# Optimization experiments

Measured on AMD Instinct MI355X. Metric: run time of the kernel, lower is better.

## Reference

```python
import jax, jax.numpy as jnp
import numpy as np

B, N, C, CODE, DIRB = 4, 321408, 3, 7, 2
K_PRE, K_POST = 1000, 300
IOU_THR, SCORE_THR, DIR_OFFSET = 0.5, 0.05, 0.0
POST_RANGE = np.array([0.0, -39.68, -5.0, 69.12, 39.68, 5.0], dtype=np.float32)


def setup_inputs() -> dict:
    key = jax.random.key(0)
    k1, k2, k3, k4 = jax.random.split(key, 4)
    box_preds = jax.random.normal(k1, (B, N, CODE), jnp.float32) * 0.3
    # shift logits down so sigmoid scores straddle the 0.05 threshold realistically
    cls_preds = jax.random.normal(k2, (B, N, C), jnp.float32) * 2.0 - 2.0
    dir_preds = jax.random.normal(k3, (B, N, DIRB), jnp.float32)
    ka, kb, kc = jax.random.split(k4, 3)
    xy = jax.random.uniform(ka, (N, 2), jnp.float32) * jnp.array([69.12, 79.36], jnp.float32) + jnp.array([0.0, -39.68], jnp.float32)
    z = jnp.full((N, 1), -1.0, jnp.float32)
    dims = jax.random.uniform(kb, (N, 3), jnp.float32, minval=1.0, maxval=4.0)
    rot = jax.random.randint(kc, (N, 1), 0, 2).astype(jnp.float32) * np.float32(np.pi / 2)
    anchors = jnp.concatenate([xy, z, dims, rot], axis=-1)
    return {"box_preds": box_preds, "cls_preds": cls_preds, "dir_preds": dir_preds, "anchors": anchors}


def _decode(deltas, anchors):
    # SECOND / PointPillars GroundBox3dCoder decode. anchors: [x,y,z,w,l,h,r]
    xa, ya, za, wa, la, ha, ra = (anchors[..., i] for i in range(7))
    xt, yt, zt, wt, lt, ht, rt = (deltas[..., i] for i in range(7))
    za = za + ha * 0.5
    diag = jnp.sqrt(la * la + wa * wa)
    xg = xt * diag + xa
    yg = yt * diag + ya
    zg = zt * ha + za
    wg = jnp.exp(wt) * wa
    lg = jnp.exp(lt) * la
    hg = jnp.exp(ht) * ha
    zg = zg - hg * 0.5
    rg = rt + ra
    return jnp.stack([xg, yg, zg, wg, lg, hg, rg], axis=-1)


def _nms_single(boxes7, scores, valid):
    # boxes_for_nms = box[:, [0,1,3,4,-1]] -> rotated (x,y,w,l,r); standup AABB of corners
    x, y, w, l, r = boxes7[:, 0], boxes7[:, 1], boxes7[:, 3], boxes7[:, 4], boxes7[:, 6]
    c, s = jnp.abs(jnp.cos(r)), jnp.abs(jnp.sin(r))
    hx = 0.5 * (w * c + l * s)   # half-extent of rotated corners along x
    hy = 0.5 * (w * s + l * c)
    x1, x2, y1, y2 = x - hx, x + hx, y - hy, y + hy
    area = (x2 - x1) * (y2 - y1)
    ix = jnp.clip(jnp.minimum(x2[:, None], x2[None, :]) - jnp.maximum(x1[:, None], x1[None, :]), 0.0)
    iy = jnp.clip(jnp.minimum(y2[:, None], y2[None, :]) - jnp.maximum(y1[:, None], y1[None, :]), 0.0)
    inter = ix * iy
    union = area[:, None] + area[None, :] - inter
    iou = jnp.where(union > 0, inter / jnp.maximum(union, 1e-12), 0.0)
    iou = jax.lax.stop_gradient(iou)
    idxs = jnp.arange(K_PRE)

    def body(keep, i):
        sup = keep[i] & (iou[i] > IOU_THR) & (idxs > i)
        return keep & ~sup, None

    keep, _ = jax.lax.scan(body, valid, idxs)
    rank = jnp.cumsum(keep) - 1                       # rank among kept (score order)
    pos = jnp.argsort(jnp.where(keep, rank, K_PRE))   # stable: kept-in-order first
    sel = pos[:K_POST]
    return sel, keep[sel]


def reference(box_preds, cls_preds, dir_preds, anchors):
    decoded = _decode(box_preds, anchors[None, :, :])          # [B,N,7]
    probs = jax.nn.sigmoid(cls_preds)                          # [B,N,C]
    top_scores = probs.max(axis=-1)
    top_labels = probs.argmax(axis=-1).astype(jnp.int32)
    dir_labels = dir_preds.argmax(axis=-1).astype(jnp.int32)
    valid = top_scores >= SCORE_THR
    sc_masked = jnp.where(valid, top_scores, -1.0)
    sc_k, idx = jax.lax.top_k(sc_masked, K_PRE)                # [B,K_PRE]
    boxes_k = jnp.take_along_axis(decoded, idx[..., None], axis=1)
    labels_k = jnp.take_along_axis(top_labels, idx, axis=1)
    dir_k = jnp.take_along_axis(dir_labels, idx, axis=1)
    valid_k = sc_k >= SCORE_THR
    sel, keep = jax.vmap(_nms_single)(boxes_k, sc_k, valid_k)  # [B,K_POST]
    boxes = jnp.take_along_axis(boxes_k, sel[..., None], axis=1)
    scores = jnp.take_along_axis(sc_k, sel, axis=1)
    labels = jnp.take_along_axis(labels_k, sel, axis=1)
    dirs = jnp.take_along_axis(dir_k, sel, axis=1)
    # direction flip: add pi where predicted direction disagrees with yaw sign
    opp = ((boxes[..., 6] - DIR_OFFSET) > 0) ^ (dirs == 1)
    r_fixed = boxes[..., 6] + jnp.where(opp, np.float32(np.pi), np.float32(0.0))
    boxes = jnp.concatenate([boxes[..., :6], r_fixed[..., None]], axis=-1)
    # post center-range filter
    lo = jnp.asarray(POST_RANGE[:3])
    hi = jnp.asarray(POST_RANGE[3:])
    in_range = jnp.all(boxes[..., :3] >= lo, axis=-1) & jnp.all(boxes[..., :3] <= hi, axis=-1)
    valid_out = keep & in_range
    boxes = jnp.where(valid_out[..., None], boxes, 0.0)
    scores = jnp.where(valid_out, scores, 0.0)
    labels = jnp.where(valid_out, labels, 0)
    return boxes, labels, scores, valid_out
```

## Files before the change

kernel.cpp:

```cpp
#include <hip/hip_runtime.h>
#include <stdint.h>

typedef unsigned long long u64;
typedef unsigned int u32;

#define BB 4
#define NN 321408
#define K_PRE 1000
#define K_POST 300
#define CAP 4096
#define NW 16
#define SCORE_THR 0.05f
#define IOU_THR 0.5f
#define SB 314
#define CH2 1024
#define NBINS 576
#define BIN0 0xBD4Cu
#define RED 8
#define RCH 40

__device__ __forceinline__ float sigm(float x) { return 1.0f / (1.0f + expf(-x)); }

__device__ __forceinline__ u32 mkkey(float mx) {
    float s = sigm(mx);
    return (s >= SCORE_THR) ? (__float_as_uint(s) | 0x80000000u) : 0u;
}

__global__ void k_score_hist(const float* __restrict__ cls, u32* __restrict__ key, u32* __restrict__ bh) {
    __shared__ u32 h1[NBINS], h2[NBINS];
    int bb = blockIdx.x, tid = threadIdx.x;
    int b = bb / SB, c = bb % SB;
    for (int i = tid; i < NBINS; i += 256) h1[i] = 0;
    __syncthreads();
    int a0 = c * CH2 + tid * 4;
    if (a0 < NN) {
        const float4* c4 = (const float4*)(cls + ((size_t)b * NN + a0) * 3);
        float4 v0 = c4[0], v1 = c4[1], v2 = c4[2];
        uint4 o;
        o.x = mkkey(fmaxf(v0.x, fmaxf(v0.y, v0.z)));
        o.y = mkkey(fmaxf(v0.w, fmaxf(v1.x, v1.y)));
        o.z = mkkey(fmaxf(v1.z, fmaxf(v1.w, v2.x)));
        o.w = mkkey(fmaxf(v2.y, fmaxf(v2.z, v2.w)));
        *((uint4*)(key + (size_t)b * NN + a0)) = o;
        if (o.x) atomicAdd(&h1[min((o.x >> 16) - BIN0, (u32)(NBINS - 1))], 1u);
        if (o.y) atomicAdd(&h1[min((o.y >> 16) - BIN0, (u32)(NBINS - 1))], 1u);
        if (o.z) atomicAdd(&h1[min((o.z >> 16) - BIN0, (u32)(NBINS - 1))], 1u);
        if (o.w) atomicAdd(&h1[min((o.w >> 16) - BIN0, (u32)(NBINS - 1))], 1u);
    }
    __syncthreads();
    u32* src = h1; u32* dst = h2;
    for (int off = 1; off < NBINS; off <<= 1) {
        for (int i = tid; i < NBINS; i += 256)
            dst[i] = src[i] + ((i + off < NBINS) ? src[i + off] : 0u);
        __syncthreads();
        u32* t = src; src = dst; dst = t;
    }
    for (int i = tid; i < NBINS; i += 256) bh[(size_t)bb * NBINS + i] = src[i];
}

__global__ __launch_bounds__(64) void k_red(const u32* __restrict__ bh, u32* __restrict__ part) {
    int blk = blockIdx.x, tid = threadIdx.x;
    int b = blk / (RED * 9);
    int r = (blk / 9) % RED;
    int g = blk % 9;
    int f = g * 64 + tid;
    int s0 = r * RCH, s1 = s0 + RCH; if (s1 > SB) s1 = SB;
    const u32* base = bh + (size_t)(b * SB + s0) * NBINS + f;
    u32 acc = 0;
    int n = s1 - s0;
    #pragma unroll 8
    for (int s = 0; s < n; ++s) acc += base[(size_t)s * NBINS];
    part[(size_t)(b * RED + r) * NBINS + f] = acc;
}

__global__ __launch_bounds__(512) void k_scanoff(const u32* __restrict__ part, const u32* __restrict__ bh,
                                                 u32* __restrict__ thr, u32* __restrict__ boff,
                                                 u32* __restrict__ cnt) {
    __shared__ u32 tot[NBINS];
    __shared__ u32 wt[8];
    __shared__ u32 sT, starg;
    int b = blockIdx.x, tid = threadIdx.x;
    for (int f = tid; f < NBINS; f += 512) {
        u32 x = 0;
        #pragma unroll
        for (int r = 0; r < RED; ++r) x += part[(size_t)(b * RED + r) * NBINS + f];
        tot[f] = x;
    }
    __syncthreads();
    if (tid == 0) {
        u32 tv = tot[0];
        starg = (tv < K_PRE) ? tv : K_PRE;
        if (starg == 0) { sT = 0x10000u; thr[b] = 0x10000u; }
    }
    __syncthreads();
    u32 target = starg;
    if (target > 0) {
        for (int f = tid; f < NBINS; f += 512) {
            u32 cge = tot[f];
            u32 cnx = (f + 1 < NBINS) ? tot[f + 1] : 0u;
            if (cge >= target && cnx < target) { sT = BIN0 + (u32)f; thr[b] = BIN0 + (u32)f; }
        }
    }
    __syncthreads();
    u32 v = 0;
    if (target > 0 && tid < SB) {
        u32 T = sT - BIN0;
        v = bh[(size_t)(b * SB + tid) * NBINS + T];
    }
    int lane = tid & 63, wv = tid >> 6;
    u32 x = v;
    #pragma unroll
    for (int o = 1; o < 64; o <<= 1) {
        u32 y = __shfl_up(x, o);
        if (lane >= o) x += y;
    }
    if (lane == 63) wt[wv] = x;
    __syncthreads();
    u32 pre = 0;
    #pragma unroll
    for (int w = 0; w < 7; ++w) pre += (w < wv) ? wt[w] : 0u;
    if (tid < SB) boff[b * SB + tid] = pre + x - v;
    if (tid == 511) cnt[b] = pre + x;
}

__global__ void k_scatter(const u32* __restrict__ key, const u32* __restrict__ thr,
                          const u32* __restrict__ boff, u64* __restrict__ cand) {
    __shared__ u32 wtot[4];
    int bb = blockIdx.x, tid = threadIdx.x;
    int b = bb / SB, c = bb % SB;
    u32 T = thr[b];
    int a0 = c * CH2 + tid * 4;
    uint4 kk = make_uint4(0u, 0u, 0u, 0u);
    if (a0 < NN) kk = *((const uint4*)(key + (size_t)b * NN + a0));
    u32 ks[4] = {kk.x, kk.y, kk.z, kk.w};
    u32 f[4];
    #pragma unroll
    for (int e = 0; e < 4; ++e) f[e] = (u32)((ks[e] != 0) && ((ks[e] >> 16) >= T));
    u32 tc = f[0] + f[1] + f[2] + f[3];
    int lane = tid & 63, wv = tid >> 6;
    u32 x = tc;
    #pragma unroll
    for (int o = 1; o < 64; o <<= 1) {
        u32 y = __shfl_up(x, o);
        if (lane >= o) x += y;
    }
    if (lane == 63) wtot[wv] = x;
    __syncthreads();
    u32 base = 0;
    u32 w0 = wtot[0], w1 = wtot[1], w2 = wtot[2];
    if (wv > 0) base += w0;
    if (wv > 1) base += w1;
    if (wv > 2) base += w2;
    u32 pos = boff[bb] + base + x - tc;
    u64* cb = cand + (size_t)b * CAP;
    #pragma unroll
    for (int e = 0; e < 4; ++e) {
        if (f[e]) {
            if (pos < CAP) cb[pos] = ((u64)(~ks[e]) << 32) | (u64)(a0 + e);
            ++pos;
        }
    }
}

__global__ __launch_bounds__(256) void k_rankdec(const u32* __restrict__ cnt, const u64* __restrict__ cand,
                                                 const float* __restrict__ boxp, const float* __restrict__ cls,
                                                 const float* __restrict__ dirp, const float* __restrict__ anch,
                                                 float* __restrict__ tks, u32* __restrict__ meta,
                                                 float* __restrict__ box7, float* __restrict__ cor) {
    __shared__ u64 ck[CAP];
    int blk = blockIdx.x, tid = threadIdx.x;
    int b = blk >> 4, rb = blk & 15;
    u32 nc = cnt[b]; if (nc > CAP) nc = CAP;
    int ci = rb * 256 + tid;
    if (rb * 256 >= (int)nc && rb * 256 >= K_PRE) return;
    const u64* cb = cand + (size_t)b * CAP;
    for (int i = tid; i < (int)nc; i += 256) ck[i] = cb[i];
    __syncthreads();

    int rank = -1; u32 idx = 0xFFFFFFFFu;
    if (ci < (int)nc) {
        u64 my = ck[ci];
        u32 r = 0;
        int j = 0;
        int nlim = (int)nc & ~15;
        for (; j < nlim; j += 16) {
            u64 v0 = ck[j+0], v1 = ck[j+1], v2 = ck[j+2], v3 = ck[j+3];
            u64 v4 = ck[j+4], v5 = ck[j+5], v6 = ck[j+6], v7 = ck[j+7];
            u64 v8 = ck[j+8], v9 = ck[j+9], va = ck[j+10], vb = ck[j+11];
            u64 vc = ck[j+12], vd = ck[j+13], ve = ck[j+14], vf = ck[j+15];
            r += (u32)(v0 < my) + (u32)(v1 < my) + (u32)(v2 < my) + (u32)(v3 < my)
               + (u32)(v4 < my) + (u32)(v5 < my) + (u32)(v6 < my) + (u32)(v7 < my)
               + (u32)(v8 < my) + (u32)(v9 < my) + (u32)(va < my) + (u32)(vb < my)
               + (u32)(vc < my) + (u32)(vd < my) + (u32)(ve < my) + (u32)(vf < my);
        }
        for (; j < (int)nc; ++j) r += (u32)(ck[j] < my);
        if (r < K_PRE) { rank = (int)r; idx = (u32)my; }
    } else if (ci < K_PRE) {
        rank = ci;
    }
    if (rank < 0) return;

    float ob[7] = {0,0,0,0,0,0,0};
    float c5[5] = {0,0,0,0,0};
    float sc = 0.f; u32 mt = 0;
    if (idx != 0xFFFFFFFFu) {
        const float* A = anch + (size_t)idx * 7;
        const float* D = boxp + ((size_t)b * NN + idx) * 7;
        float xa=A[0], ya=A[1], za=A[2], wa=A[3], la=A[4], ha=A[5], ra=A[6];
        float xt=D[0], yt=D[1], zt=D[2], wt=D[3], lt=D[4], ht=D[5], rt=D[6];
        za = za + ha * 0.5f;
        float diag = sqrtf(la * la + wa * wa);
        float xg = xt * diag + xa;
        float yg = yt * diag + ya;
        float zg = zt * ha + za;
        float wg = expf(wt) * wa;
        float lg = expf(lt) * la;
        float hg = expf(ht) * ha;
        zg = zg - hg * 0.5f;
        float rg = rt + ra;
        ob[0]=xg; ob[1]=yg; ob[2]=zg; ob[3]=wg; ob[4]=lg; ob[5]=hg; ob[6]=rg;
        float cr = fabsf(cosf(rg)), sr = fabsf(sinf(rg));
        float hx = 0.5f * (wg * cr + lg * sr);
        float hy = 0.5f * (wg * sr + lg * cr);
        float x1 = xg - hx, x2 = xg + hx, y1 = yg - hy, y2 = yg + hy;
        c5[0]=x1; c5[1]=x2; c5[2]=y1; c5[3]=y2; c5[4]=(x2-x1)*(y2-y1);
        const float* cc = cls + ((size_t)b * NN + idx) * 3;
        float p0 = sigm(cc[0]), p1 = sigm(cc[1]), p2 = sigm(cc[2]);
        int lbl = 0; float best = p0;
        if (p1 > best) { best = p1; lbl = 1; }
        if (p2 > best) { best = p2; lbl = 2; }
        sc = best;
        const float* dd = dirp + ((size_t)b * NN + idx) * 2;
        int dl = (dd[1] > dd[0]) ? 1 : 0;
        mt = (u32)lbl | ((u32)dl << 8) | (1u << 16);
    }
    size_t t = (size_t)b * K_PRE + rank;
    tks[t] = sc; meta[t] = mt;
    #pragma unroll
    for (int j = 0; j < 7; ++j) box7[t * 7 + j] = ob[j];
    #pragma unroll
    for (int j = 0; j < 5; ++j) cor[t * 5 + j] = c5[j];
}

__global__ __launch_bounds__(256) void k_maskT(const float* __restrict__ cor, u64* __restrict__ maskT) {
    __shared__ float s4[(K_PRE + 16) * 4];
    __shared__ float sA[K_PRE + 16];
    int blk = blockIdx.x;
    int b = blk / 63, jb = blk % 63;
    int tid = threadIdx.x;
    const float4* C4 = (const float4*)(cor + (size_t)b * K_PRE * 5);
    for (int q = tid; q < (K_PRE * 5) / 4; q += 256) {
        float4 v = C4[q];
        int t0 = q * 4;
        #pragma unroll
        for (int e = 0; e < 4; ++e) {
            int t = t0 + e;
            int i = t / 5, k = t - i * 5;
            float val = (e == 0) ? v.x : (e == 1) ? v.y : (e == 2) ? v.z : v.w;
            int ip = i + (i >> 6);
            if (k < 4) s4[ip * 4 + k] = val; else sA[ip] = val;
        }
    }
    __syncthreads();
    int w = tid & 15, jl = tid >> 4;
    int j = jb * 16 + jl;
    if (j >= K_PRE) return;
    int jp = j + (j >> 6);
    float x1 = s4[jp*4+0], x2 = s4[jp*4+1], y1 = s4[jp*4+2], y2 = s4[jp*4+3], ar = sA[jp];
    u64 m = 0;
    int i0 = w * 64;
    if (i0 < j) {
        int iend = j - i0; if (iend > 64) iend = 64;
        for (int ii = 0; ii < iend; ++ii) {
            int i = i0 + ii;
            int ip = i + (i >> 6);
            float4 bx = *(const float4*)&s4[ip * 4];
            float ai = sA[ip];
            float ix = fminf(x2, bx.y) - fmaxf(x1, bx.x); ix = fmaxf(ix, 0.f);
            float iy = fminf(y2, bx.w) - fmaxf(y1, bx.z); iy = fmaxf(iy, 0.f);
            float inter = ix * iy;
            float uni = ai + ar - inter;
            float iou = (uni > 0.f) ? inter / fmaxf(uni, 1e-12f) : 0.f;
            if (iou > IOU_THR) m |= (1ull << ii);
        }
    }
    maskT[((size_t)b * K_PRE + j) * NW + w] = m;
}

__global__ __launch_bounds__(256) void k_nms_out(const u32* __restrict__ meta, const float* __restrict__ box7,
                                                 const float* __restrict__ tks, const u64* __restrict__ maskT,
                                                 float* __restrict__ out) {
    int b = blockIdx.x; int tid = threadIdx.x;
    __shared__ u64 km_s[16];
    __shared__ int sel_s[K_POST];
    __shared__ int cnt_s;
    if (tid < 16) km_s[tid] = 0ull;
    __syncthreads();
    if (tid < 64) {
        int lane = tid;
        const u32* M = meta + b * K_PRE;
        int cnt = 0; bool done = false;
        for (int c = 0; c < 16; ++c) {
            if (done) break;
            int j = c * 64 + lane;
            int jc = (j < K_PRE) ? j : (K_PRE - 1);
            bool jvalid = (j < K_PRE) && ((M[jc] >> 16) & 1u);
            const u64* colp = maskT + ((size_t)b * K_PRE + jc) * NW;
            u64 cw = 0; u64 supacc = 0;
            #pragma unroll
            for (int w = 0; w < 16; ++w) {
                u64 cv = colp[w];
                supacc |= (cv & km_s[w]);
                if (w == c) cw = cv;
            }
            u64 active = __ballot(jvalid && (supacc == 0ull));
            u64 kmc = 0;
            while (active) {
                int i = __ffsll((unsigned long long)active) - 1;
                if (lane == 0) sel_s[cnt] = c * 64 + i;
                ++cnt;
                if (cnt >= K_POST) { done = true; break; }
                kmc |= (1ull << i);
                u64 supb = __ballot(((cw >> i) & 1ull) != 0ull);
                active &= ~supb;
                active &= ~(1ull << i);
            }
            if (lane == 0) km_s[c] = kmc;
        }
        if (lane == 0) cnt_s = cnt;
    }
    __syncthreads();
    int cnt = cnt_s;
    const u32* M = meta + b * K_PRE;
    const float* BX = box7 + (size_t)b * K_PRE * 7;
    const float* SS = tks + b * K_PRE;
    for (int p = tid; p < K_POST; p += 256) {
        float ob[7] = {0,0,0,0,0,0,0};
        float sc = 0.f, lb = 0.f, vd = 0.f;
        if (p < cnt) {
            int i = sel_s[p];
            float xg = BX[i*7+0], yg = BX[i*7+1], zg = BX[i*7+2];
            bool in_range = (xg >= 0.0f) && (xg <= 69.12f) &&
                            (yg >= -39.68f) && (yg <= 39.68f) &&
                            (zg >= -5.0f) && (zg <= 5.0f);
            if (in_range) {
                u32 mt = M[i];
                int dl = (mt >> 8) & 0xFF;
                float r = BX[i*7+6];
                bool opp = ((r > 0.0f) != (dl == 1));
                float rf = r + (opp ? 3.14159274f : 0.0f);
                ob[0]=xg; ob[1]=yg; ob[2]=zg; ob[3]=BX[i*7+3]; ob[4]=BX[i*7+4]; ob[5]=BX[i*7+5]; ob[6]=rf;
                sc = SS[i]; lb = (float)(mt & 0xFF); vd = 1.0f;
            }
        }
        size_t ro = (size_t)(b * K_POST + p);
        #pragma unroll
        for (int j = 0; j < 7; ++j) out[ro * 7 + j] = ob[j];
        out[(size_t)BB * K_POST * 7 + ro] = lb;
        out[(size_t)BB * K_POST * 8 + ro] = sc;
        out[(size_t)BB * K_POST * 9 + ro] = vd;
    }
}

extern "C" void kernel_launch(void* const* d_in, const int* in_sizes, int n_in,
                              void* d_out, int out_size, void* d_ws, size_t ws_size,
                              hipStream_t stream) {
    const float* boxp = (const float*)d_in[0];
    const float* cls  = (const float*)d_in[1];
    const float* dirp = (const float*)d_in[2];
    const float* anch = (const float*)d_in[3];
    float* out = (float*)d_out;

    char* p = (char*)d_ws;
    u32* key  = (u32*)p; p += (size_t)BB * NN * 4;
    u32* bh   = (u32*)p; p += (size_t)BB * SB * NBINS * 4;
    u32* part = (u32*)p; p += (size_t)BB * RED * NBINS * 4;
    u32* cnt  = (u32*)p; p += 256;
    u32* thr  = (u32*)p; p += 256;
    u32* boff = (u32*)p; p += (size_t)BB * SB * 4 + 256;
    u64* cand = (u64*)p; p += (size_t)BB * CAP * 8;
    float* tks = (float*)p; p += (size_t)BB * K_PRE * 4;
    u32* meta = (u32*)p; p += (size_t)BB * K_PRE * 4;
    float* box7 = (float*)p; p += (size_t)BB * K_PRE * 7 * 4;
    float* cor  = (float*)p; p += (size_t)BB * K_PRE * 5 * 4;
    u64* maskT = (u64*)p; p += (size_t)BB * K_PRE * NW * 8;

    k_score_hist<<<BB * SB, 256, 0, stream>>>(cls, key, bh);
    k_red<<<BB * RED * 9, 64, 0, stream>>>(bh, part);
    k_scanoff<<<BB, 512, 0, stream>>>(part, bh, thr, boff, cnt);
    k_scatter<<<BB * SB, 256, 0, stream>>>(key, thr, boff, cand);
    k_rankdec<<<BB * 16, 256, 0, stream>>>(cnt, cand, boxp, cls, dirp, anch, tks, meta, box7, cor);
    k_maskT<<<BB * 63, 256, 0, stream>>>(cor, maskT);
    k_nms_out<<<BB, 256, 0, stream>>>(meta, box7, tks, maskT, out);
}
```

Before: 87.91 us.

## Fuse all pipeline stages into one cooperative persistent kernel with grid syncs

```diff
diff --git a/kernel.cpp b/kernel.cpp
--- a/kernel.cpp
+++ b/kernel.cpp
@@ -1,5 +1,8 @@
 #include <hip/hip_runtime.h>
+#include <hip/hip_cooperative_groups.h>
 #include <stdint.h>
+
+namespace cg = cooperative_groups;
 
 typedef unsigned long long u64;
 typedef unsigned int u32;
@@ -18,12 +21,369 @@
 #define BIN0 0xBD4Cu
 #define RED 8
 #define RCH 40
+#define GRID 256
+#define TPB 256
 
 __device__ __forceinline__ float sigm(float x) { return 1.0f / (1.0f + expf(-x)); }
 
 __device__ __forceinline__ u32 mkkey(float mx) {
     float s = sigm(mx);
     return (s >= SCORE_THR) ? (__float_as_uint(s) | 0x80000000u) : 0u;
+}
+
+struct P1s { u32 h1[NBINS]; u32 h2[NBINS]; };
+struct P3s { u32 tot[NBINS]; u32 wt[4]; u32 sT; u32 starg; };
+struct P4s { u32 wtot[4]; };
+struct P5s { u64 ck[CAP]; };
+struct P6s { float s4[(K_PRE + 16) * 4]; float sA[K_PRE + 16]; };
+struct P7s { u64 km[16]; int sel[K_POST]; int cnt_s; };
+union SmemU { P1s p1; P3s p3; P4s p4; P5s p5; P6s p6; P7s p7; };
+
+__global__ void __launch_bounds__(TPB) k_mega(const float* __restrict__ boxp, const float* __restrict__ cls,
+                                              const float* __restrict__ dirp, const float* __restrict__ anch,
+                                              float* __restrict__ out, char* __restrict__ ws) {
+    __shared__ SmemU sm;
+    cg::grid_group gg = cg::this_grid();
+    int bid = blockIdx.x, tid = threadIdx.x;
+    int lane = tid & 63, wv = tid >> 6;
+
+    char* p = ws;
+    u32* key  = (u32*)p; p += (size_t)BB * NN * 4;
+    u32* bh   = (u32*)p; p += (size_t)BB * SB * NBINS * 4;
+    u32* part = (u32*)p; p += (size_t)BB * RED * NBINS * 4;
+    u32* cnt  = (u32*)p; p += 256;
+    u32* thr  = (u32*)p; p += 256;
+    u32* boff = (u32*)p; p += (size_t)BB * SB * 4 + 256;
+    u64* cand = (u64*)p; p += (size_t)BB * CAP * 8;
+    float* tks = (float*)p; p += (size_t)BB * K_PRE * 4;
+    u32* meta = (u32*)p; p += (size_t)BB * K_PRE * 4;
+    float* box7 = (float*)p; p += (size_t)BB * K_PRE * 7 * 4;
+    float* cor  = (float*)p; p += (size_t)BB * K_PRE * 5 * 4;
+    u64* maskT = (u64*)p;
+
+    for (int task = bid; task < BB * SB; task += GRID) {
+        int b = task / SB, c = task % SB;
+        for (int i = tid; i < NBINS; i += TPB) sm.p1.h1[i] = 0;
+        __syncthreads();
+        int a0 = c * CH2 + tid * 4;
+        if (a0 < NN) {
+            const float4* c4 = (const float4*)(cls + ((size_t)b * NN + a0) * 3);
+            float4 v0 = c4[0], v1 = c4[1], v2 = c4[2];
+            uint4 o;
+            o.x = mkkey(fmaxf(v0.x, fmaxf(v0.y, v0.z)));
+            o.y = mkkey(fmaxf(v0.w, fmaxf(v1.x, v1.y)));
+            o.z = mkkey(fmaxf(v1.z, fmaxf(v1.w, v2.x)));
+            o.w = mkkey(fmaxf(v2.y, fmaxf(v2.z, v2.w)));
+            *((uint4*)(key + (size_t)b * NN + a0)) = o;
+            if (o.x) atomicAdd(&sm.p1.h1[min((o.x >> 16) - BIN0, (u32)(NBINS - 1))], 1u);
+            if (o.y) atomicAdd(&sm.p1.h1[min((o.y >> 16) - BIN0, (u32)(NBINS - 1))], 1u);
+            if (o.z) atomicAdd(&sm.p1.h1[min((o.z >> 16) - BIN0, (u32)(NBINS - 1))], 1u);
+            if (o.w) atomicAdd(&sm.p1.h1[min((o.w >> 16) - BIN0, (u32)(NBINS - 1))], 1u);
+        }
+        __syncthreads();
+        u32* src = sm.p1.h1; u32* dst = sm.p1.h2;
+        for (int off = 1; off < NBINS; off <<= 1) {
+            for (int i = tid; i < NBINS; i += TPB)
+                dst[i] = src[i] + ((i + off < NBINS) ? src[i + off] : 0u);
+            __syncthreads();
+            u32* t = src; src = dst; dst = t;
+        }
+        for (int i = tid; i < NBINS; i += TPB) bh[(size_t)task * NBINS + i] = src[i];
+        __syncthreads();
+    }
+    gg.sync();
+
+    if (bid < BB * RED * 3) {
+        int b = bid / (RED * 3), r = (bid / 3) % RED, g = bid % 3;
+        int f = g * 256 + tid;
+        if (f < NBINS) {
+            int s0 = r * RCH, s1 = s0 + RCH; if (s1 > SB) s1 = SB;
+            const u32* base = bh + (size_t)(b * SB + s0) * NBINS + f;
+            u32 acc = 0; int n = s1 - s0;
+            #pragma unroll 8
+            for (int s = 0; s < n; ++s) acc += base[(size_t)s * NBINS];
+            part[(size_t)(b * RED + r) * NBINS + f] = acc;
+        }
+    }
+    gg.sync();
+
+    if (bid < BB) {
+        int b = bid;
+        for (int f = tid; f < NBINS; f += TPB) {
+            u32 x = 0;
+            #pragma unroll
+            for (int r = 0; r < RED; ++r) x += part[(size_t)(b * RED + r) * NBINS + f];
+            sm.p3.tot[f] = x;
+        }
+        __syncthreads();
+        if (tid == 0) {
+            u32 tv = sm.p3.tot[0];
+            sm.p3.starg = (tv < K_PRE) ? tv : K_PRE;
+            if (sm.p3.starg == 0) { sm.p3.sT = 0x10000u; thr[b] = 0x10000u; }
+        }
+        __syncthreads();
+        u32 target = sm.p3.starg;
+        if (target > 0) {
+            for (int f = tid; f < NBINS; f += TPB) {
+                u32 cge = sm.p3.tot[f];
+                u32 cnx = (f + 1 < NBINS) ? sm.p3.tot[f + 1] : 0u;
+                if (cge >= target && cnx < target) { sm.p3.sT = BIN0 + (u32)f; thr[b] = BIN0 + (u32)f; }
+            }
+        }
+        __syncthreads();
+        u32 T = sm.p3.sT;
+        u32 vA = 0, vB = 0;
+        if (target > 0) {
+            if (tid < SB) vA = bh[(size_t)(b * SB + tid) * NBINS + (T - BIN0)];
+            if (tid + 256 < SB) vB = bh[(size_t)(b * SB + tid + 256) * NBINS + (T - BIN0)];
+        }
+        u32 x = vA;
+        #pragma unroll
+        for (int o = 1; o < 64; o <<= 1) { u32 y = __shfl_up(x, o); if (lane >= o) x += y; }
+        if (lane == 63) sm.p3.wt[wv] = x;
+        __syncthreads();
+        u32 preA = 0, totA;
+        { u32 w0 = sm.p3.wt[0], w1 = sm.p3.wt[1], w2 = sm.p3.wt[2], w3 = sm.p3.wt[3];
+          if (wv > 0) preA += w0; if (wv > 1) preA += w1; if (wv > 2) preA += w2;
+          totA = w0 + w1 + w2 + w3; }
+        __syncthreads();
+        u32 xb = vB;
+        #pragma unroll
+        for (int o = 1; o < 64; o <<= 1) { u32 y = __shfl_up(xb, o); if (lane >= o) xb += y; }
+        if (lane == 63) sm.p3.wt[wv] = xb;
+        __syncthreads();
+        u32 preB = 0, totB;
+        { u32 w0 = sm.p3.wt[0], w1 = sm.p3.wt[1], w2 = sm.p3.wt[2], w3 = sm.p3.wt[3];
+          if (wv > 0) preB += w0; if (wv > 1) preB += w1; if (wv > 2) preB += w2;
+          totB = w0 + w1 + w2 + w3; }
+        if (tid < SB) boff[b * SB + tid] = preA + x - vA;
+        if (tid + 256 < SB) boff[b * SB + tid + 256] = totA + preB + xb - vB;
+        if (tid == 0) cnt[b] = totA + totB;
+    }
+    gg.sync();
+
+    for (int task = bid; task < BB * SB; task += GRID) {
+        int b = task / SB, c = task % SB;
+        u32 T = thr[b];
+        int a0 = c * CH2 + tid * 4;
+        uint4 kk = make_uint4(0u, 0u, 0u, 0u);
+        if (a0 < NN) kk = *((const uint4*)(key + (size_t)b * NN + a0));
+        u32 ks[4] = {kk.x, kk.y, kk.z, kk.w};
+        u32 f[4];
+        #pragma unroll
+        for (int e = 0; e < 4; ++e) f[e] = (u32)((ks[e] != 0) && ((ks[e] >> 16) >= T));
+        u32 tc = f[0] + f[1] + f[2] + f[3];
+        u32 x = tc;
+        #pragma unroll
+        for (int o = 1; o < 64; o <<= 1) { u32 y = __shfl_up(x, o); if (lane >= o) x += y; }
+        if (lane == 63) sm.p4.wtot[wv] = x;
+        __syncthreads();
+        u32 base = 0;
+        { u32 w0 = sm.p4.wtot[0], w1 = sm.p4.wtot[1], w2 = sm.p4.wtot[2];
+          if (wv > 0) base += w0; if (wv > 1) base += w1; if (wv > 2) base += w2; }
+        u32 pos = boff[task] + base + x - tc;
+        u64* cb = cand + (size_t)b * CAP;
+        #pragma unroll
+        for (int e = 0; e < 4; ++e) {
+            if (f[e]) {
+                if (pos < CAP) cb[pos] = ((u64)(~ks[e]) << 32) | (u64)(a0 + e);
+                ++pos;
+            }
+        }
+        __syncthreads();
+    }
+    gg.sync();
+
+    {
+        int b = bid >> 6, g = bid & 63;
+        u32 nc = cnt[b]; if (nc > CAP) nc = CAP;
+        int ci0 = g * 64;
+        bool active = (ci0 < (int)nc) || (ci0 < K_PRE);
+        if (active) {
+            const u64* cb = cand + (size_t)b * CAP;
+            for (int i = tid; i < (int)nc; i += TPB) sm.p5.ck[i] = cb[i];
+            __syncthreads();
+            int rank = -1; u32 idx = 0xFFFFFFFFu;
+            if (tid < 64) {
+                int ci = ci0 + tid;
+                if (ci < (int)nc) {
+                    u64 my = sm.p5.ck[ci];
+                    u32 r = 0;
+                    int j = 0, nlim = (int)nc & ~15;
+                    for (; j < nlim; j += 16) {
+                        u64 v0 = sm.p5.ck[j+0], v1 = sm.p5.ck[j+1], v2 = sm.p5.ck[j+2], v3 = sm.p5.ck[j+3];
+                        u64 v4 = sm.p5.ck[j+4], v5 = sm.p5.ck[j+5], v6 = sm.p5.ck[j+6], v7 = sm.p5.ck[j+7];
+                        u64 v8 = sm.p5.ck[j+8], v9 = sm.p5.ck[j+9], va = sm.p5.ck[j+10], vb = sm.p5.ck[j+11];
+                        u64 vc = sm.p5.ck[j+12], vd = sm.p5.ck[j+13], ve = sm.p5.ck[j+14], vf = sm.p5.ck[j+15];
+                        r += (u32)(v0 < my) + (u32)(v1 < my) + (u32)(v2 < my) + (u32)(v3 < my)
+                           + (u32)(v4 < my) + (u32)(v5 < my) + (u32)(v6 < my) + (u32)(v7 < my)
+                           + (u32)(v8 < my) + (u32)(v9 < my) + (u32)(va < my) + (u32)(vb < my)
+                           + (u32)(vc < my) + (u32)(vd < my) + (u32)(ve < my) + (u32)(vf < my);
+                    }
+                    for (; j < (int)nc; ++j) r += (u32)(sm.p5.ck[j] < my);
+                    if (r < K_PRE) { rank = (int)r; idx = (u32)my; }
+                } else if (ci < K_PRE) {
+                    rank = ci;
+                }
+            }
+            if (rank >= 0) {
+                float ob[7] = {0,0,0,0,0,0,0};
+                float c5[5] = {0,0,0,0,0};
+                float sc = 0.f; u32 mt = 0;
+                if (idx != 0xFFFFFFFFu) {
+                    const float* A = anch + (size_t)idx * 7;
+                    const float* D = boxp + ((size_t)b * NN + idx) * 7;
+                    float xa=A[0], ya=A[1], za=A[2], wa=A[3], la=A[4], ha=A[5], ra=A[6];
+                    float xt=D[0], yt=D[1], zt=D[2], wt2=D[3], lt=D[4], ht=D[5], rt=D[6];
+                    za = za + ha * 0.5f;
+                    float diag = sqrtf(la * la + wa * wa);
+                    float xg = xt * diag + xa;
+                    float yg = yt * diag + ya;
+                    float zg = zt * ha + za;
+                    float wg = expf(wt2) * wa;
+                    float lg = expf(lt) * la;
+                    float hg = expf(ht) * ha;
+                    zg = zg - hg * 0.5f;
+                    float rg = rt + ra;
+                    ob[0]=xg; ob[1]=yg; ob[2]=zg; ob[3]=wg; ob[4]=lg; ob[5]=hg; ob[6]=rg;
+                    float cr = fabsf(cosf(rg)), sr = fabsf(sinf(rg));
+                    float hx = 0.5f * (wg * cr + lg * sr);
+                    float hy = 0.5f * (wg * sr + lg * cr);
+                    float x1 = xg - hx, x2 = xg + hx, y1 = yg - hy, y2 = yg + hy;
+                    c5[0]=x1; c5[1]=x2; c5[2]=y1; c5[3]=y2; c5[4]=(x2-x1)*(y2-y1);
+                    const float* cc = cls + ((size_t)b * NN + idx) * 3;
+                    float p0 = sigm(cc[0]), p1 = sigm(cc[1]), p2 = sigm(cc[2]);
+                    int lbl = 0; float best = p0;
+                    if (p1 > best) { best = p1; lbl = 1; }
+                    if (p2 > best) { best = p2; lbl = 2; }
+                    sc = best;
+                    const float* dd = dirp + ((size_t)b * NN + idx) * 2;
+                    int dl = (dd[1] > dd[0]) ? 1 : 0;
+                    mt = (u32)lbl | ((u32)dl << 8) | (1u << 16);
+                }
+                size_t t = (size_t)b * K_PRE + rank;
+                tks[t] = sc; meta[t] = mt;
+                #pragma unroll
+                for (int j = 0; j < 7; ++j) box7[t * 7 + j] = ob[j];
+                #pragma unroll
+                for (int j = 0; j < 5; ++j) cor[t * 5 + j] = c5[j];
+            }
+        }
+    }
+    gg.sync();
+
+    if (bid < BB * 63) {
+        int b = bid / 63, jb = bid % 63;
+        const float4* C4 = (const float4*)(cor + (size_t)b * K_PRE * 5);
+        for (int q = tid; q < (K_PRE * 5) / 4; q += TPB) {
+            float4 v = C4[q];
+            int t0 = q * 4;
+            #pragma unroll
+            for (int e = 0; e < 4; ++e) {
+                int t = t0 + e;
+                int i = t / 5, k = t - i * 5;
+                float val = (e == 0) ? v.x : (e == 1) ? v.y : (e == 2) ? v.z : v.w;
+                int ip = i + (i >> 6);
+                if (k < 4) sm.p6.s4[ip * 4 + k] = val; else sm.p6.sA[ip] = val;
+            }
+        }
+        __syncthreads();
+        int w = tid & 15, jl = tid >> 4;
+        int j = jb * 16 + jl;
+        if (j < K_PRE) {
+            int jp = j + (j >> 6);
+            float x1 = sm.p6.s4[jp*4+0], x2 = sm.p6.s4[jp*4+1];
+            float y1 = sm.p6.s4[jp*4+2], y2 = sm.p6.s4[jp*4+3], ar = sm.p6.sA[jp];
+            u64 m = 0;
+            int i0 = w * 64;
+            if (i0 < j) {
+                int iend = j - i0; if (iend > 64) iend = 64;
+                for (int ii = 0; ii < iend; ++ii) {
+                    int i = i0 + ii;
+                    int ip = i + (i >> 6);
+                    float4 bx = *(const float4*)&sm.p6.s4[ip * 4];
+                    float ai = sm.p6.sA[ip];
+                    float ix = fminf(x2, bx.y) - fmaxf(x1, bx.x); ix = fmaxf(ix, 0.f);
+                    float iy = fminf(y2, bx.w) - fmaxf(y1, bx.z); iy = fmaxf(iy, 0.f);
+                    float inter = ix * iy;
+                    float uni = ai + ar - inter;
+                    float iou = (uni > 0.f) ? inter / fmaxf(uni, 1e-12f) : 0.f;
+                    if (iou > IOU_THR) m |= (1ull << ii);
+                }
+            }
+            maskT[((size_t)b * K_PRE + j) * NW + w] = m;
+        }
+    }
+    gg.sync();
+
+    if (bid < BB) {
+        int b = bid;
+        if (tid < 16) sm.p7.km[tid] = 0ull;
+        __syncthreads();
+        if (tid < 64) {
+            int c2 = 0; bool done = false;
+            const u32* M = meta + b * K_PRE;
+            for (int c = 0; c < 16; ++c) {
+                if (done) break;
+                int j = c * 64 + lane;
+                int jc = (j < K_PRE) ? j : (K_PRE - 1);
+                bool jvalid = (j < K_PRE) && ((M[jc] >> 16) & 1u);
+                const u64* colp = maskT + ((size_t)b * K_PRE + jc) * NW;
+                u64 cw = 0; u64 supacc = 0;
+                #pragma unroll
+                for (int w = 0; w < 16; ++w) {
+                    u64 cv = colp[w];
+                    supacc |= (cv & sm.p7.km[w]);
+                    if (w == c) cw = cv;
+                }
+                u64 active2 = __ballot(jvalid && (supacc == 0ull));
+                u64 kmc = 0;
+                while (active2) {
+                    int i = __ffsll((unsigned long long)active2) - 1;
+                    if (lane == 0) sm.p7.sel[c2] = c * 64 + i;
+                    ++c2;
+                    if (c2 >= K_POST) { done = true; break; }
+                    kmc |= (1ull << i);
+                    u64 supb = __ballot(((cw >> i) & 1ull) != 0ull);
+                    active2 &= ~supb;
+                    active2 &= ~(1ull << i);
+                }
+                if (lane == 0) sm.p7.km[c] = kmc;
+            }
+            if (lane == 0) sm.p7.cnt_s = c2;
+        }
+        __syncthreads();
+        int kept = sm.p7.cnt_s;
+        const u32* M = meta + b * K_PRE;
+        const float* BX = box7 + (size_t)b * K_PRE * 7;
+        const float* SS = tks + b * K_PRE;
+        for (int pp = tid; pp < K_POST; pp += TPB) {
+            float ob[7] = {0,0,0,0,0,0,0};
+            float sc = 0.f, lb = 0.f, vd = 0.f;
+            if (pp < kept) {
+                int i = sm.p7.sel[pp];
+                float xg = BX[i*7+0], yg = BX[i*7+1], zg = BX[i*7+2];
+                bool in_range = (xg >= 0.0f) && (xg <= 69.12f) &&
+                                (yg >= -39.68f) && (yg <= 39.68f) &&
+                                (zg >= -5.0f) && (zg <= 5.0f);
+                if (in_range) {
+                    u32 mt = M[i];
+                    int dl = (mt >> 8) & 0xFF;
+                    float r = BX[i*7+6];
+                    bool opp = ((r > 0.0f) != (dl == 1));
+                    float rf = r + (opp ? 3.14159274f : 0.0f);
+                    ob[0]=xg; ob[1]=yg; ob[2]=zg; ob[3]=BX[i*7+3]; ob[4]=BX[i*7+4]; ob[5]=BX[i*7+5]; ob[6]=rf;
+                    sc = SS[i]; lb = (float)(mt & 0xFF); vd = 1.0f;
+                }
+            }
+            size_t ro = (size_t)(b * K_POST + pp);
+            #pragma unroll
+            for (int j = 0; j < 7; ++j) out[ro * 7 + j] = ob[j];
+            out[(size_t)BB * K_POST * 7 + ro] = lb;
+            out[(size_t)BB * K_POST * 8 + ro] = sc;
+            out[(size_t)BB * K_POST * 9 + ro] = vd;
+        }
+    }
 }
 
 __global__ void k_score_hist(const float* __restrict__ cls, u32* __restrict__ key, u32* __restrict__ bh) {
@@ -60,14 +420,11 @@
 
 __global__ __launch_bounds__(64) void k_red(const u32* __restrict__ bh, u32* __restrict__ part) {
     int blk = blockIdx.x, tid = threadIdx.x;
-    int b = blk / (RED * 9);
-    int r = (blk / 9) % RED;
-    int g = blk % 9;
+    int b = blk / (RED * 9); int r = (blk / 9) % RED; int g = blk % 9;
     int f = g * 64 + tid;
     int s0 = r * RCH, s1 = s0 + RCH; if (s1 > SB) s1 = SB;
     const u32* base = bh + (size_t)(b * SB + s0) * NBINS + f;
-    u32 acc = 0;
-    int n = s1 - s0;
+    u32 acc = 0; int n = s1 - s0;
     #pragma unroll 8
     for (int s = 0; s < n; ++s) acc += base[(size_t)s * NBINS];
     part[(size_t)(b * RED + r) * NBINS + f] = acc;
@@ -103,17 +460,11 @@
     }
     __syncthreads();
     u32 v = 0;
-    if (target > 0 && tid < SB) {
-        u32 T = sT - BIN0;
-        v = bh[(size_t)(b * SB + tid) * NBINS + T];
-    }
+    if (target > 0 && tid < SB) v = bh[(size_t)(b * SB + tid) * NBINS + (sT - BIN0)];
     int lane = tid & 63, wv = tid >> 6;
     u32 x = v;
     #pragma unroll
-    for (int o = 1; o < 64; o <<= 1) {
-        u32 y = __shfl_up(x, o);
-        if (lane >= o) x += y;
-    }
+    for (int o = 1; o < 64; o <<= 1) { u32 y = __shfl_up(x, o); if (lane >= o) x += y; }
     if (lane == 63) wt[wv] = x;
     __syncthreads();
     u32 pre = 0;
@@ -140,10 +491,7 @@
     int lane = tid & 63, wv = tid >> 6;
     u32 x = tc;
     #pragma unroll
-    for (int o = 1; o < 64; o <<= 1) {
-        u32 y = __shfl_up(x, o);
-        if (lane >= o) x += y;
-    }
+    for (int o = 1; o < 64; o <<= 1) { u32 y = __shfl_up(x, o); if (lane >= o) x += y; }
     if (lane == 63) wtot[wv] = x;
     __syncthreads();
     u32 base = 0;
@@ -176,13 +524,11 @@
     const u64* cb = cand + (size_t)b * CAP;
     for (int i = tid; i < (int)nc; i += 256) ck[i] = cb[i];
     __syncthreads();
-
     int rank = -1; u32 idx = 0xFFFFFFFFu;
     if (ci < (int)nc) {
         u64 my = ck[ci];
         u32 r = 0;
-        int j = 0;
-        int nlim = (int)nc & ~15;
+        int j = 0, nlim = (int)nc & ~15;
         for (; j < nlim; j += 16) {
             u64 v0 = ck[j+0], v1 = ck[j+1], v2 = ck[j+2], v3 = ck[j+3];
             u64 v4 = ck[j+4], v5 = ck[j+5], v6 = ck[j+6], v7 = ck[j+7];
@@ -199,7 +545,6 @@
         rank = ci;
     }
     if (rank < 0) return;
-
     float ob[7] = {0,0,0,0,0,0,0};
     float c5[5] = {0,0,0,0,0};
     float sc = 0.f; u32 mt = 0;
@@ -370,26 +715,32 @@
     const float* dirp = (const float*)d_in[2];
     const float* anch = (const float*)d_in[3];
     float* out = (float*)d_out;
-
-    char* p = (char*)d_ws;
-    u32* key  = (u32*)p; p += (size_t)BB * NN * 4;
-    u32* bh   = (u32*)p; p += (size_t)BB * SB * NBINS * 4;
-    u32* part = (u32*)p; p += (size_t)BB * RED * NBINS * 4;
-    u32* cnt  = (u32*)p; p += 256;
-    u32* thr  = (u32*)p; p += 256;
-    u32* boff = (u32*)p; p += (size_t)BB * SB * 4 + 256;
-    u64* cand = (u64*)p; p += (size_t)BB * CAP * 8;
-    float* tks = (float*)p; p += (size_t)BB * K_PRE * 4;
-    u32* meta = (u32*)p; p += (size_t)BB * K_PRE * 4;
-    float* box7 = (float*)p; p += (size_t)BB * K_PRE * 7 * 4;
-    float* cor  = (float*)p; p += (size_t)BB * K_PRE * 5 * 4;
-    u64* maskT = (u64*)p; p += (size_t)BB * K_PRE * NW * 8;
-
-    k_score_hist<<<BB * SB, 256, 0, stream>>>(cls, key, bh);
-    k_red<<<BB * RED * 9, 64, 0, stream>>>(bh, part);
-    k_scanoff<<<BB, 512, 0, stream>>>(part, bh, thr, boff, cnt);
-    k_scatter<<<BB * SB, 256, 0, stream>>>(key, thr, boff, cand);
-    k_rankdec<<<BB * 16, 256, 0, stream>>>(cnt, cand, boxp, cls, dirp, anch, tks, meta, box7, cor);
-    k_maskT<<<BB * 63, 256, 0, stream>>>(cor, maskT);
-    k_nms_out<<<BB, 256, 0, stream>>>(meta, box7, tks, maskT, out);
-}
+    char* ws = (char*)d_ws;
+
+    void* args[] = { (void*)&boxp, (void*)&cls, (void*)&dirp, (void*)&anch, (void*)&out, (void*)&ws };
+    hipError_t err = hipLaunchCooperativeKernel((const void*)k_mega, dim3(GRID), dim3(TPB),
+                                                (void**)args, 0, stream);
+    if (err != hipSuccess) {
+        char* p = ws;
+        u32* key  = (u32*)p; p += (size_t)BB * NN * 4;
+        u32* bh   = (u32*)p; p += (size_t)BB * SB * NBINS * 4;
+        u32* part = (u32*)p; p += (size_t)BB * RED * NBINS * 4;
+        u32* cnt  = (u32*)p; p += 256;
+        u32* thr  = (u32*)p; p += 256;
+        u32* boff = (u32*)p; p += (size_t)BB * SB * 4 + 256;
+        u64* cand = (u64*)p; p += (size_t)BB * CAP * 8;
+        float* tks = (float*)p; p += (size_t)BB * K_PRE * 4;
+        u32* meta = (u32*)p; p += (size_t)BB * K_PRE * 4;
+        float* box7 = (float*)p; p += (size_t)BB * K_PRE * 7 * 4;
+        float* cor  = (float*)p; p += (size_t)BB * K_PRE * 5 * 4;
+        u64* maskT = (u64*)p;
+
+        k_score_hist<<<BB * SB, 256, 0, stream>>>(cls, key, bh);
+        k_red<<<BB * RED * 9, 64, 0, stream>>>(bh, part);
+        k_scanoff<<<BB, 512, 0, stream>>>(part, bh, thr, boff, cnt);
+        k_scatter<<<BB * SB, 256, 0, stream>>>(key, thr, boff, cand);
+        k_rankdec<<<BB * 16, 256, 0, stream>>>(cnt, cand, boxp, cls, dirp, anch, tks, meta, box7, cor);
+        k_maskT<<<BB * 63, 256, 0, stream>>>(cor, maskT);
+        k_nms_out<<<BB, 256, 0, stream>>>(meta, box7, tks, maskT, out);
+    }
+}
```

New measurement: 259.8 us. 2.96x slower.

## Fuse threshold scan and bucket-offset prefix into scatter kernel

Applied to the files above, without the earlier changes.

```diff
diff --git a/kernel.cpp b/kernel.cpp
--- a/kernel.cpp
+++ b/kernel.cpp
@@ -73,71 +73,54 @@
     part[(size_t)(b * RED + r) * NBINS + f] = acc;
 }
 
-__global__ __launch_bounds__(512) void k_scanoff(const u32* __restrict__ part, const u32* __restrict__ bh,
-                                                 u32* __restrict__ thr, u32* __restrict__ boff,
-                                                 u32* __restrict__ cnt) {
+__global__ __launch_bounds__(256) void k_scatterT(const u32* __restrict__ key, const u32* __restrict__ part,
+                                                  const u32* __restrict__ bh, u32* __restrict__ cnt,
+                                                  u64* __restrict__ cand) {
     __shared__ u32 tot[NBINS];
-    __shared__ u32 wt[8];
-    __shared__ u32 sT, starg;
-    int b = blockIdx.x, tid = threadIdx.x;
-    for (int f = tid; f < NBINS; f += 512) {
+    __shared__ u32 wtot[4];
+    __shared__ u32 sTf;
+    int bb = blockIdx.x, tid = threadIdx.x;
+    int b = bb / SB, c = bb % SB;
+    int lane = tid & 63, wv = tid >> 6;
+    for (int f = tid; f < NBINS; f += 256) {
         u32 x = 0;
         #pragma unroll
         for (int r = 0; r < RED; ++r) x += part[(size_t)(b * RED + r) * NBINS + f];
         tot[f] = x;
     }
     __syncthreads();
-    if (tid == 0) {
-        u32 tv = tot[0];
-        starg = (tv < K_PRE) ? tv : K_PRE;
-        if (starg == 0) { sT = 0x10000u; thr[b] = 0x10000u; }
-    }
-    __syncthreads();
-    u32 target = starg;
-    if (target > 0) {
-        for (int f = tid; f < NBINS; f += 512) {
-            u32 cge = tot[f];
-            u32 cnx = (f + 1 < NBINS) ? tot[f + 1] : 0u;
-            if (cge >= target && cnx < target) { sT = BIN0 + (u32)f; thr[b] = BIN0 + (u32)f; }
-        }
-    }
-    __syncthreads();
-    u32 v = 0;
-    if (target > 0 && tid < SB) {
-        u32 T = sT - BIN0;
-        v = bh[(size_t)(b * SB + tid) * NBINS + T];
-    }
-    int lane = tid & 63, wv = tid >> 6;
-    u32 x = v;
-    #pragma unroll
-    for (int o = 1; o < 64; o <<= 1) {
-        u32 y = __shfl_up(x, o);
-        if (lane >= o) x += y;
-    }
-    if (lane == 63) wt[wv] = x;
-    __syncthreads();
-    u32 pre = 0;
-    #pragma unroll
-    for (int w = 0; w < 7; ++w) pre += (w < wv) ? wt[w] : 0u;
-    if (tid < SB) boff[b * SB + tid] = pre + x - v;
-    if (tid == 511) cnt[b] = pre + x;
-}
-
-__global__ void k_scatter(const u32* __restrict__ key, const u32* __restrict__ thr,
-                          const u32* __restrict__ boff, u64* __restrict__ cand) {
-    __shared__ u32 wtot[4];
-    int bb = blockIdx.x, tid = threadIdx.x;
-    int b = bb / SB, c = bb % SB;
-    u32 T = thr[b];
+    u32 tv = tot[0];
+    u32 target = (tv < K_PRE) ? tv : K_PRE;
+    if (target == 0) {
+        if (c == 0 && tid == 0) cnt[b] = 0;
+        return;
+    }
+    for (int f = tid; f < NBINS; f += 256) {
+        u32 cge = tot[f];
+        u32 cnx = (f + 1 < NBINS) ? tot[f + 1] : 0u;
+        if (cge >= target && cnx < target) sTf = (u32)f;
+    }
+    __syncthreads();
+    u32 Tf = sTf;
+    if (c == 0 && tid == 0) cnt[b] = tot[Tf];
+    u32 m = 0;
+    if (tid < c) m = bh[(size_t)(b * SB + tid) * NBINS + Tf];
+    if (tid + 256 < c) m += bh[(size_t)(b * SB + tid + 256) * NBINS + Tf];
+    #pragma unroll
+    for (int o = 32; o > 0; o >>= 1) m += __shfl_down(m, o);
+    if (lane == 0) wtot[wv] = m;
+    __syncthreads();
+    u32 boffc = wtot[0] + wtot[1] + wtot[2] + wtot[3];
+    __syncthreads();
+    u32 T16 = BIN0 + Tf;
     int a0 = c * CH2 + tid * 4;
     uint4 kk = make_uint4(0u, 0u, 0u, 0u);
     if (a0 < NN) kk = *((const uint4*)(key + (size_t)b * NN + a0));
     u32 ks[4] = {kk.x, kk.y, kk.z, kk.w};
-    u32 f[4];
-    #pragma unroll
-    for (int e = 0; e < 4; ++e) f[e] = (u32)((ks[e] != 0) && ((ks[e] >> 16) >= T));
-    u32 tc = f[0] + f[1] + f[2] + f[3];
-    int lane = tid & 63, wv = tid >> 6;
+    u32 f4[4];
+    #pragma unroll
+    for (int e = 0; e < 4; ++e) f4[e] = (u32)((ks[e] != 0) && ((ks[e] >> 16) >= T16));
+    u32 tc = f4[0] + f4[1] + f4[2] + f4[3];
     u32 x = tc;
     #pragma unroll
     for (int o = 1; o < 64; o <<= 1) {
@@ -147,15 +130,13 @@
     if (lane == 63) wtot[wv] = x;
     __syncthreads();
     u32 base = 0;
-    u32 w0 = wtot[0], w1 = wtot[1], w2 = wtot[2];
-    if (wv > 0) base += w0;
-    if (wv > 1) base += w1;
-    if (wv > 2) base += w2;
-    u32 pos = boff[bb] + base + x - tc;
+    { u32 w0 = wtot[0], w1 = wtot[1], w2 = wtot[2];
+      if (wv > 0) base += w0; if (wv > 1) base += w1; if (wv > 2) base += w2; }
+    u32 pos = boffc + base + x - tc;
     u64* cb = cand + (size_t)b * CAP;
     #pragma unroll
     for (int e = 0; e < 4; ++e) {
-        if (f[e]) {
+        if (f4[e]) {
             if (pos < CAP) cb[pos] = ((u64)(~ks[e]) << 32) | (u64)(a0 + e);
             ++pos;
         }
@@ -376,8 +357,6 @@
     u32* bh   = (u32*)p; p += (size_t)BB * SB * NBINS * 4;
     u32* part = (u32*)p; p += (size_t)BB * RED * NBINS * 4;
     u32* cnt  = (u32*)p; p += 256;
-    u32* thr  = (u32*)p; p += 256;
-    u32* boff = (u32*)p; p += (size_t)BB * SB * 4 + 256;
     u64* cand = (u64*)p; p += (size_t)BB * CAP * 8;
     float* tks = (float*)p; p += (size_t)BB * K_PRE * 4;
     u32* meta = (u32*)p; p += (size_t)BB * K_PRE * 4;
@@ -387,8 +366,7 @@
 
     k_score_hist<<<BB * SB, 256, 0, stream>>>(cls, key, bh);
     k_red<<<BB * RED * 9, 64, 0, stream>>>(bh, part);
-    k_scanoff<<<BB, 512, 0, stream>>>(part, bh, thr, boff, cnt);
-    k_scatter<<<BB * SB, 256, 0, stream>>>(key, thr, boff, cand);
+    k_scatterT<<<BB * SB, 256, 0, stream>>>(key, part, bh, cnt, cand);
     k_rankdec<<<BB * 16, 256, 0, stream>>>(cnt, cand, boxp, cls, dirp, anch, tks, meta, box7, cor);
     k_maskT<<<BB * 63, 256, 0, stream>>>(cor, maskT);
     k_nms_out<<<BB, 256, 0, stream>>>(meta, box7, tks, maskT, out);
```

Result: no change. 87.15 us (-0.9%).
